# Kernel tuning notes

Hardware: AMD Instinct MI355X
Metric: run time of the kernel (lower is better)

Reference implementation:

```python
import jax, jax.numpy as jnp
import numpy as np

I = 512   # input_size (acts as the row/batch dim)
H = 512   # hidden_size
T = 256   # time steps
STDV = 1.0 / float(np.sqrt(H))


def setup_inputs() -> dict:
    key = jax.random.key(0)
    ks = jax.random.split(key, 20)
    u = lambda k, shape: jax.random.uniform(k, shape, jnp.float32, -STDV, STDV)
    data = jax.random.normal(ks[0], (6, T, I, 1), jnp.float32)
    data = data.at[1].set((data[1] > 0.0).astype(jnp.float32))  # m: binary observation mask
    data = data.at[2].set(jnp.abs(data[2]))                     # d: nonnegative time deltas
    state = jax.random.normal(ks[1], (I, H), jnp.float32) * 0.1
    return dict(
        data=data, state=state,
        w_dg_x=u(ks[2], (I, 1)), w_dg_h=u(ks[3], (1, H)),
        w_xr=u(ks[4], (1, H)), w_hr=u(ks[5], (H, H)), w_mr=u(ks[6], (1, H)),
        w_xz=u(ks[7], (1, H)), w_hz=u(ks[8], (H, H)), w_mz=u(ks[9], (1, H)),
        w_xh=u(ks[10], (1, H)), w_hh=u(ks[11], (H, H)), w_mh=u(ks[12], (1, H)),
        b_dg_x=u(ks[13], (I, 1)), b_dg_h=u(ks[14], (I, H)),
        b_r=u(ks[15], (I, H)), b_z=u(ks[16], (I, H)), b_h=u(ks[17], (I, H)),
    )


def reference(data, state, w_dg_x, w_dg_h, w_xr, w_hr, w_mr, w_xz, w_hz, w_mz,
              w_xh, w_hh, w_mh, b_dg_x, b_dg_h, b_r, b_z, b_h):
    # GRU-D 'mloss' branch; Dropout layer is identity at inference (training=None).
    def step(h, xs):
        x, m, d, xpie = xs  # each (I, 1)
        gamma_x = jnp.exp(-jax.nn.relu(w_dg_x * d + b_dg_x))        # (I, 1)
        gamma_h = jnp.exp(-jax.nn.relu(d @ w_dg_h + b_dg_h))        # (I, H)
        x = m * x + (1.0 - m) * (gamma_x * xpie)                    # decay-gated imputation
        h = gamma_h * h
        r = jax.nn.sigmoid(x @ w_xr + h @ w_hr + m @ w_mr + b_r)    # (I, H)
        z = jax.nn.sigmoid(x @ w_xz + h @ w_hz + m @ w_mz + b_z)
        h_tilde = jnp.tanh(x @ w_xh + (r * h) @ w_hh + m @ w_mh + b_h)
        h_new = (1.0 - z) * h + z * h_tilde
        return h_new, h_new

    _, states = jax.lax.scan(step, state, (data[0], data[1], data[2], data[3]))
    return states  # (T, I, H) hidden state per timestep
```

## Files before the change

kernel.cpp:

```cpp
#include <hip/hip_runtime.h>

typedef _Float16 f16;
typedef _Float16 f16x8 __attribute__((ext_vector_type(8)));
typedef float f32x4 __attribute__((ext_vector_type(4)));

#define T_STEPS 256
#define I_DIM   512
#define H_DIM   512
#define TI      (T_STEPS * I_DIM)
#define ROWS    16
#define NPW     32
#define PADC    520
#define MATSZ   262144

__global__ __launch_bounds__(256) void prep_weights(
    const float* __restrict__ w_hr, const float* __restrict__ w_hz,
    const float* __restrict__ w_hh, f16* __restrict__ wf)
{
    int idx = blockIdx.x * 256 + threadIdx.x;
    int mat = idx >> 18;
    int r   = idx & (MATSZ - 1);
    int nt  = r >> 13;
    int r1  = r & 8191;
    int kk  = r1 >> 9;
    int r2  = r1 & 511;
    int l   = r2 >> 3;
    int j   = r2 & 7;
    int k = kk * 32 + ((l >> 4) << 3) + j;
    int n = (nt << 4) + (l & 15);
    const float* W = (mat == 0) ? w_hr : (mat == 1) ? w_hz : w_hh;
    wf[idx] = (f16)W[k * H_DIM + n];
}

__global__ __launch_bounds__(1024) void grud_main(
    const float* __restrict__ data, const float* __restrict__ state,
    const float* __restrict__ w_dg_x, const float* __restrict__ w_dg_h,
    const float* __restrict__ w_xr, const float* __restrict__ w_mr,
    const float* __restrict__ w_xz, const float* __restrict__ w_mz,
    const float* __restrict__ w_xh, const float* __restrict__ w_mh,
    const float* __restrict__ b_dg_x, const float* __restrict__ b_dg_h,
    const float* __restrict__ b_r, const float* __restrict__ b_z,
    const float* __restrict__ b_h,
    const f16* __restrict__ wf, float* __restrict__ out)
{
    __shared__ f16 hdec_l[ROWS][PADC];
    __shared__ f16 rh_l[ROWS][PADC];

    const int tid = threadIdx.x;
    const int w   = tid >> 6;
    const int l   = tid & 63;
    const int lhi = l >> 4;
    const int llo = l & 15;
    const int n0  = w * NPW;
    const int rowbase = blockIdx.x * ROWS;

    const f16* wfr = wf + (size_t)(2 * w) * 8192;
    const f16* wfz = wfr + MATSZ;
    const f16* wfh = wfr + 2 * MATSZ;

    float h_reg[4][2];
    float hdec[4][2];
    float zreg[4][2];
    float ximp[4], mval[4];

#pragma unroll
    for (int reg = 0; reg < 4; ++reg) {
        int gi = rowbase + lhi * 4 + reg;
#pragma unroll
        for (int c = 0; c < 2; ++c)
            h_reg[reg][c] = state[(size_t)gi * H_DIM + n0 + llo + 16 * c];
    }

    for (int t = 0; t < T_STEPS; ++t) {
#pragma unroll
        for (int reg = 0; reg < 4; ++reg) {
            int i  = lhi * 4 + reg;
            int gi = rowbase + i;
            float d  = data[2 * TI + t * I_DIM + gi];
            float m  = data[1 * TI + t * I_DIM + gi];
            float x  = data[0 * TI + t * I_DIM + gi];
            float xp = data[3 * TI + t * I_DIM + gi];
            float gx = __expf(-fmaxf(w_dg_x[gi] * d + b_dg_x[gi], 0.0f));
            ximp[reg] = m * x + (1.0f - m) * (gx * xp);
            mval[reg] = m;
#pragma unroll
            for (int c = 0; c < 2; ++c) {
                int n = n0 + llo + 16 * c;
                float gh = __expf(-fmaxf(d * w_dg_h[n] + b_dg_h[(size_t)gi * H_DIM + n], 0.0f));
                float hd = gh * h_reg[reg][c];
                hdec[reg][c] = hd;
                hdec_l[i][n] = (f16)hd;
            }
        }
        __syncthreads();

        f32x4 acc_r0 = {0.f,0.f,0.f,0.f}, acc_r1 = {0.f,0.f,0.f,0.f};
        f32x4 acc_z0 = {0.f,0.f,0.f,0.f}, acc_z1 = {0.f,0.f,0.f,0.f};
#pragma unroll
        for (int kk = 0; kk < 16; ++kk) {
            f16x8 a = *(const f16x8*)&hdec_l[llo][kk * 32 + lhi * 8];
            const int fo = (kk * 64 + l) * 8;
            f16x8 br0 = *(const f16x8*)(wfr + fo);
            f16x8 br1 = *(const f16x8*)(wfr + 8192 + fo);
            f16x8 bz0 = *(const f16x8*)(wfz + fo);
            f16x8 bz1 = *(const f16x8*)(wfz + 8192 + fo);
            acc_r0 = __builtin_amdgcn_mfma_f32_16x16x32_f16(a, br0, acc_r0, 0, 0, 0);
            acc_r1 = __builtin_amdgcn_mfma_f32_16x16x32_f16(a, br1, acc_r1, 0, 0, 0);
            acc_z0 = __builtin_amdgcn_mfma_f32_16x16x32_f16(a, bz0, acc_z0, 0, 0, 0);
            acc_z1 = __builtin_amdgcn_mfma_f32_16x16x32_f16(a, bz1, acc_z1, 0, 0, 0);
        }
#pragma unroll
        for (int reg = 0; reg < 4; ++reg) {
            int i  = lhi * 4 + reg;
            int gi = rowbase + i;
#pragma unroll
            for (int c = 0; c < 2; ++c) {
                int n = n0 + llo + 16 * c;
                float sr = (c ? acc_r1[reg] : acc_r0[reg])
                         + ximp[reg] * w_xr[n] + mval[reg] * w_mr[n]
                         + b_r[(size_t)gi * H_DIM + n];
                float rr = 1.0f / (1.0f + __expf(-sr));
                float sz = (c ? acc_z1[reg] : acc_z0[reg])
                         + ximp[reg] * w_xz[n] + mval[reg] * w_mz[n]
                         + b_z[(size_t)gi * H_DIM + n];
                zreg[reg][c] = 1.0f / (1.0f + __expf(-sz));
                rh_l[i][n] = (f16)(rr * hdec[reg][c]);
            }
        }
        __syncthreads();

        f32x4 acc_h0 = {0.f,0.f,0.f,0.f}, acc_h1 = {0.f,0.f,0.f,0.f};
#pragma unroll
        for (int kk = 0; kk < 16; ++kk) {
            f16x8 a = *(const f16x8*)&rh_l[llo][kk * 32 + lhi * 8];
            const int fo = (kk * 64 + l) * 8;
            f16x8 bh0 = *(const f16x8*)(wfh + fo);
            f16x8 bh1 = *(const f16x8*)(wfh + 8192 + fo);
            acc_h0 = __builtin_amdgcn_mfma_f32_16x16x32_f16(a, bh0, acc_h0, 0, 0, 0);
            acc_h1 = __builtin_amdgcn_mfma_f32_16x16x32_f16(a, bh1, acc_h1, 0, 0, 0);
        }
#pragma unroll
        for (int reg = 0; reg < 4; ++reg) {
            int gi = rowbase + lhi * 4 + reg;
#pragma unroll
            for (int c = 0; c < 2; ++c) {
                int n = n0 + llo + 16 * c;
                float sh = (c ? acc_h1[reg] : acc_h0[reg])
                         + ximp[reg] * w_xh[n] + mval[reg] * w_mh[n]
                         + b_h[(size_t)gi * H_DIM + n];
                float e  = __expf(2.0f * sh);
                float th = 1.0f - 2.0f / (e + 1.0f);
                float hn = (1.0f - zreg[reg][c]) * hdec[reg][c] + zreg[reg][c] * th;
                h_reg[reg][c] = hn;
                out[((size_t)t * I_DIM + gi) * H_DIM + n] = hn;
            }
        }
    }
}

extern "C" void kernel_launch(void* const* d_in, const int* in_sizes, int n_in,
                              void* d_out, int out_size, void* d_ws, size_t ws_size,
                              hipStream_t stream) {
    const float* data   = (const float*)d_in[0];
    const float* state  = (const float*)d_in[1];
    const float* w_dg_x = (const float*)d_in[2];
    const float* w_dg_h = (const float*)d_in[3];
    const float* w_xr   = (const float*)d_in[4];
    const float* w_hr   = (const float*)d_in[5];
    const float* w_mr   = (const float*)d_in[6];
    const float* w_xz   = (const float*)d_in[7];
    const float* w_hz   = (const float*)d_in[8];
    const float* w_mz   = (const float*)d_in[9];
    const float* w_xh   = (const float*)d_in[10];
    const float* w_hh   = (const float*)d_in[11];
    const float* w_mh   = (const float*)d_in[12];
    const float* b_dg_x = (const float*)d_in[13];
    const float* b_dg_h = (const float*)d_in[14];
    const float* b_r    = (const float*)d_in[15];
    const float* b_z    = (const float*)d_in[16];
    const float* b_h    = (const float*)d_in[17];
    f16* wf = (f16*)d_ws;
    float* out = (float*)d_out;

    prep_weights<<<3072, 256, 0, stream>>>(w_hr, w_hz, w_hh, wf);
    grud_main<<<32, 1024, 0, stream>>>(data, state, w_dg_x, w_dg_h,
        w_xr, w_mr, w_xz, w_mz, w_xh, w_mh,
        b_dg_x, b_dg_h, b_r, b_z, b_h, wf, out);
}
```

Before: 11.86 ms.

## Split GRU-D hidden columns across 256 blocks with flag-based inter-block sync

```diff
diff --git a/kernel.cpp b/kernel.cpp
--- a/kernel.cpp
+++ b/kernel.cpp
@@ -1,17 +1,30 @@
 #include <hip/hip_runtime.h>
 
 typedef _Float16 f16;
+typedef _Float16 f16x2 __attribute__((ext_vector_type(2)));
 typedef _Float16 f16x8 __attribute__((ext_vector_type(8)));
 typedef float f32x4 __attribute__((ext_vector_type(4)));
+typedef unsigned int uint32;
 
 #define T_STEPS 256
 #define I_DIM   512
 #define H_DIM   512
 #define TI      (T_STEPS * I_DIM)
+#define MATSZ   262144
 #define ROWS    16
-#define NPW     32
+#define COLS    64
 #define PADC    520
-#define MATSZ   262144
+#define NBLK    256
+
+#define WF_BYTES  (3 * MATSZ * 2)
+#define HX_OFF    WF_BYTES
+#define HX_BYTES  (2 * NBLK * ROWS * COLS * 4)
+#define RHX_OFF   (HX_OFF + HX_BYTES)
+#define RHX_BYTES (2 * NBLK * (ROWS/2) * COLS * 4)
+#define FLAG_OFF  (RHX_OFF + RHX_BYTES)
+#define FLAG_INTS (NBLK * 2 * 16)
+
+#define SCOPE_AGENT __HIP_MEMORY_SCOPE_AGENT
 
 __global__ __launch_bounds__(256) void prep_weights(
     const float* __restrict__ w_hr, const float* __restrict__ w_hz,
@@ -32,7 +45,21 @@
     wf[idx] = (f16)W[k * H_DIM + n];
 }
 
-__global__ __launch_bounds__(1024) void grud_main(
+__global__ __launch_bounds__(256) void init_flags(int* flags)
+{
+    for (int i = threadIdx.x; i < FLAG_INTS; i += 256) flags[i] = 0;
+}
+
+__device__ inline void spin_ge(int* f, int tgt)
+{
+    long guard = 0;
+    while (__hip_atomic_load(f, __ATOMIC_ACQUIRE, SCOPE_AGENT) < tgt) {
+        __builtin_amdgcn_s_sleep(8);
+        if (++guard > 500000) break;
+    }
+}
+
+__global__ __launch_bounds__(256, 1) void grud_main(
     const float* __restrict__ data, const float* __restrict__ state,
     const float* __restrict__ w_dg_x, const float* __restrict__ w_dg_h,
     const float* __restrict__ w_xr, const float* __restrict__ w_mr,
@@ -41,120 +68,214 @@
     const float* __restrict__ b_dg_x, const float* __restrict__ b_dg_h,
     const float* __restrict__ b_r, const float* __restrict__ b_z,
     const float* __restrict__ b_h,
-    const f16* __restrict__ wf, float* __restrict__ out)
+    char* __restrict__ ws, float* __restrict__ out)
 {
-    __shared__ f16 hdec_l[ROWS][PADC];
-    __shared__ f16 rh_l[ROWS][PADC];
+    const f16*   wf   = (const f16*)ws;
+    float*       hxf  = (float*)(ws + HX_OFF);
+    uint32*      rhx  = (uint32*)(ws + RHX_OFF);
+    int*         flags= (int*)(ws + FLAG_OFF);
+
+    __shared__ f16   a_l[ROWS][PADC];
+    __shared__ float hdecf[ROWS][COLS + 4];
+    __shared__ float wdh_l[H_DIM];
+    __shared__ float wcol[6][COLS];
+    __shared__ float brl[ROWS][COLS + 4], bzl[ROWS][COLS + 4], bhl[ROWS][COLS + 4];
+    __shared__ float dvl[ROWS], ximpl[ROWS], mvl[ROWS];
+    __shared__ float wdx_l[ROWS], bdx_l[ROWS];
 
     const int tid = threadIdx.x;
-    const int w   = tid >> 6;
+    const int wv  = tid >> 6;
     const int l   = tid & 63;
     const int lhi = l >> 4;
     const int llo = l & 15;
-    const int n0  = w * NPW;
-    const int rowbase = blockIdx.x * ROWS;
-
-    const f16* wfr = wf + (size_t)(2 * w) * 8192;
-    const f16* wfz = wfr + MATSZ;
-    const f16* wfh = wfr + 2 * MATSZ;
-
-    float h_reg[4][2];
-    float hdec[4][2];
-    float zreg[4][2];
-    float ximp[4], mval[4];
-
-#pragma unroll
-    for (int reg = 0; reg < 4; ++reg) {
-        int gi = rowbase + lhi * 4 + reg;
-#pragma unroll
-        for (int c = 0; c < 2; ++c)
-            h_reg[reg][c] = state[(size_t)gi * H_DIM + n0 + llo + 16 * c];
-    }
+    const int rg  = blockIdx.x >> 3;
+    const int cg  = blockIdx.x & 7;
+    const int rowbase = rg * ROWS;
+    const int s_own   = blockIdx.x;
+    int* flag_h_own  = flags + (s_own * 2 + 0) * 16;
+    int* flag_rh_own = flags + (s_own * 2 + 1) * 16;
+
+    f16x8 wr[16], wz[16], wh[16];
+    {
+        const f16* wfb = wf + (size_t)(cg * 4 + wv) * 8192;
+#pragma unroll
+        for (int kk = 0; kk < 16; ++kk) {
+            wr[kk] = *(const f16x8*)(wfb + (kk * 64 + l) * 8);
+            wz[kk] = *(const f16x8*)(wfb + MATSZ + (kk * 64 + l) * 8);
+            wh[kk] = *(const f16x8*)(wfb + 2 * MATSZ + (kk * 64 + l) * 8);
+        }
+    }
+
+    for (int idx = tid; idx < H_DIM; idx += 256) wdh_l[idx] = w_dg_h[idx];
+    for (int idx = tid; idx < 6 * COLS; idx += 256) {
+        int mat = idx >> 6, c = idx & 63;
+        const float* src = (mat == 0) ? w_xr : (mat == 1) ? w_mr : (mat == 2) ? w_xz
+                          : (mat == 3) ? w_mz : (mat == 4) ? w_xh : w_mh;
+        wcol[mat][c] = src[cg * 64 + c];
+    }
+    for (int idx = tid; idx < 3 * ROWS * COLS; idx += 256) {
+        int which = idx >> 10, r = (idx >> 6) & 15, c = idx & 63;
+        const float* src = (which == 0) ? b_r : (which == 1) ? b_z : b_h;
+        float v = src[(size_t)(rowbase + r) * H_DIM + cg * 64 + c];
+        if (which == 0) brl[r][c] = v; else if (which == 1) bzl[r][c] = v; else bhl[r][c] = v;
+    }
+    if (tid < ROWS) {
+        wdx_l[tid] = w_dg_x[rowbase + tid];
+        bdx_l[tid] = b_dg_x[rowbase + tid];
+    }
+    __syncthreads();
+
+    const int di = tid & 15;
+    const int dq = tid >> 4;
+
+    float zsave[4];
 
     for (int t = 0; t < T_STEPS; ++t) {
-#pragma unroll
-        for (int reg = 0; reg < 4; ++reg) {
-            int i  = lhi * 4 + reg;
-            int gi = rowbase + i;
-            float d  = data[2 * TI + t * I_DIM + gi];
-            float m  = data[1 * TI + t * I_DIM + gi];
-            float x  = data[0 * TI + t * I_DIM + gi];
+        if (tid == 0 && t > 0) {
+            __threadfence();
+            __hip_atomic_store(flag_h_own, t, __ATOMIC_RELEASE, SCOPE_AGENT);
+            for (int p = 1; p < 8; ++p) {
+                int cgp = (cg + p) & 7;
+                spin_ge(flags + ((rg * 8 + cgp) * 2 + 0) * 16, t);
+            }
+        }
+        if (tid >= 16 && tid < 32) {
+            int i2 = tid - 16;
+            int gi = rowbase + i2;
+            float dd = data[2 * TI + t * I_DIM + gi];
+            float mm = data[1 * TI + t * I_DIM + gi];
+            float xx = data[0 * TI + t * I_DIM + gi];
             float xp = data[3 * TI + t * I_DIM + gi];
-            float gx = __expf(-fmaxf(w_dg_x[gi] * d + b_dg_x[gi], 0.0f));
-            ximp[reg] = m * x + (1.0f - m) * (gx * xp);
-            mval[reg] = m;
-#pragma unroll
-            for (int c = 0; c < 2; ++c) {
-                int n = n0 + llo + 16 * c;
-                float gh = __expf(-fmaxf(d * w_dg_h[n] + b_dg_h[(size_t)gi * H_DIM + n], 0.0f));
-                float hd = gh * h_reg[reg][c];
-                hdec[reg][c] = hd;
-                hdec_l[i][n] = (f16)hd;
-            }
-        }
-        __syncthreads();
-
-        f32x4 acc_r0 = {0.f,0.f,0.f,0.f}, acc_r1 = {0.f,0.f,0.f,0.f};
-        f32x4 acc_z0 = {0.f,0.f,0.f,0.f}, acc_z1 = {0.f,0.f,0.f,0.f};
+            float gx = __expf(-fmaxf(wdx_l[i2] * dd + bdx_l[i2], 0.0f));
+            dvl[i2] = dd; mvl[i2] = mm;
+            ximpl[i2] = mm * xx + (1.0f - mm) * gx * xp;
+        }
+        __syncthreads();
+
+        {
+            float dd = dvl[di];
+#pragma unroll
+            for (int half = 0; half < 2; ++half) {
+                int k0 = dq * 32 + half * 16;
+                int cgp = k0 >> 6, nb = k0 & 63;
+                float hv[16];
+                if (t == 0) {
+                    const float* sp = state + (size_t)(rowbase + di) * H_DIM + k0;
+#pragma unroll
+                    for (int j = 0; j < 16; ++j) hv[j] = sp[j];
+                } else {
+                    float* hp = hxf + ((size_t)(t & 1) * NBLK + rg * 8 + cgp) * 1024 + di * 64 + nb;
+#pragma unroll
+                    for (int j = 0; j < 16; ++j)
+                        hv[j] = __hip_atomic_load(hp + j, __ATOMIC_RELAXED, SCOPE_AGENT);
+                }
+                const float* bp = b_dg_h + (size_t)(rowbase + di) * H_DIM + k0;
+                f16 hd[16];
+                bool own = (cgp == cg);
+#pragma unroll
+                for (int j = 0; j < 16; ++j) {
+                    float g = __expf(-fmaxf(dd * wdh_l[k0 + j] + bp[j], 0.0f));
+                    float hdv = g * hv[j];
+                    hd[j] = (f16)hdv;
+                    if (own) hdecf[di][nb + j] = hdv;
+                }
+                f16x8 v0, v1;
+#pragma unroll
+                for (int j = 0; j < 8; ++j) { v0[j] = hd[j]; v1[j] = hd[8 + j]; }
+                *(f16x8*)&a_l[di][k0] = v0;
+                *(f16x8*)&a_l[di][k0 + 8] = v1;
+            }
+        }
+        __syncthreads();
+
+        f32x4 ar = {0.f, 0.f, 0.f, 0.f}, az = {0.f, 0.f, 0.f, 0.f};
 #pragma unroll
         for (int kk = 0; kk < 16; ++kk) {
-            f16x8 a = *(const f16x8*)&hdec_l[llo][kk * 32 + lhi * 8];
-            const int fo = (kk * 64 + l) * 8;
-            f16x8 br0 = *(const f16x8*)(wfr + fo);
-            f16x8 br1 = *(const f16x8*)(wfr + 8192 + fo);
-            f16x8 bz0 = *(const f16x8*)(wfz + fo);
-            f16x8 bz1 = *(const f16x8*)(wfz + 8192 + fo);
-            acc_r0 = __builtin_amdgcn_mfma_f32_16x16x32_f16(a, br0, acc_r0, 0, 0, 0);
-            acc_r1 = __builtin_amdgcn_mfma_f32_16x16x32_f16(a, br1, acc_r1, 0, 0, 0);
-            acc_z0 = __builtin_amdgcn_mfma_f32_16x16x32_f16(a, bz0, acc_z0, 0, 0, 0);
-            acc_z1 = __builtin_amdgcn_mfma_f32_16x16x32_f16(a, bz1, acc_z1, 0, 0, 0);
-        }
-#pragma unroll
-        for (int reg = 0; reg < 4; ++reg) {
-            int i  = lhi * 4 + reg;
-            int gi = rowbase + i;
-#pragma unroll
-            for (int c = 0; c < 2; ++c) {
-                int n = n0 + llo + 16 * c;
-                float sr = (c ? acc_r1[reg] : acc_r0[reg])
-                         + ximp[reg] * w_xr[n] + mval[reg] * w_mr[n]
-                         + b_r[(size_t)gi * H_DIM + n];
+            f16x8 a = *(const f16x8*)&a_l[llo][kk * 32 + lhi * 8];
+            ar = __builtin_amdgcn_mfma_f32_16x16x32_f16(a, wr[kk], ar, 0, 0, 0);
+            az = __builtin_amdgcn_mfma_f32_16x16x32_f16(a, wz[kk], az, 0, 0, 0);
+        }
+        {
+            const int n = (wv << 4) + llo;
+            uint32* rslice = rhx + ((size_t)(t & 1) * NBLK + s_own) * 512;
+            float rh[4];
+#pragma unroll
+            for (int reg = 0; reg < 4; ++reg) {
+                int i = 4 * lhi + reg;
+                float sr = ar[reg] + ximpl[i] * wcol[0][n] + mvl[i] * wcol[1][n] + brl[i][n];
                 float rr = 1.0f / (1.0f + __expf(-sr));
-                float sz = (c ? acc_z1[reg] : acc_z0[reg])
-                         + ximp[reg] * w_xz[n] + mval[reg] * w_mz[n]
-                         + b_z[(size_t)gi * H_DIM + n];
-                zreg[reg][c] = 1.0f / (1.0f + __expf(-sz));
-                rh_l[i][n] = (f16)(rr * hdec[reg][c]);
-            }
-        }
-        __syncthreads();
-
-        f32x4 acc_h0 = {0.f,0.f,0.f,0.f}, acc_h1 = {0.f,0.f,0.f,0.f};
+                float sz = az[reg] + ximpl[i] * wcol[2][n] + mvl[i] * wcol[3][n] + bzl[i][n];
+                zsave[reg] = 1.0f / (1.0f + __expf(-sz));
+                rh[reg] = rr * hdecf[i][n];
+            }
+#pragma unroll
+            for (int b = 0; b < 2; ++b) {
+                f16x2 p; p.x = (f16)rh[2 * b]; p.y = (f16)rh[2 * b + 1];
+                __hip_atomic_store(rslice + (2 * lhi + b) * 64 + n,
+                                   __builtin_bit_cast(uint32, p), __ATOMIC_RELAXED, SCOPE_AGENT);
+            }
+        }
+        __syncthreads();
+
+        if (tid == 0) {
+            __threadfence();
+            __hip_atomic_store(flag_rh_own, t + 1, __ATOMIC_RELEASE, SCOPE_AGENT);
+            for (int p = 1; p < 8; ++p) {
+                int cgp = (cg + p) & 7;
+                spin_ge(flags + ((rg * 8 + cgp) * 2 + 1) * 16, t + 1);
+            }
+        }
+        __syncthreads();
+
+        {
+            int cgp = tid >> 5, j = tid & 31;
+            int rp = j >> 2, n0 = (j & 3) * 16;
+            const uint32* src = rhx + ((size_t)(t & 1) * NBLK + rg * 8 + cgp) * 512 + rp * 64 + n0;
+            f16 lo[16], hi[16];
+#pragma unroll
+            for (int jj = 0; jj < 16; ++jj) {
+                uint32 u = __hip_atomic_load((uint32*)(src + jj), __ATOMIC_RELAXED, SCOPE_AGENT);
+                f16x2 p = __builtin_bit_cast(f16x2, u);
+                lo[jj] = p.x; hi[jj] = p.y;
+            }
+            int k0 = cgp * 64 + n0;
+            f16x8 v0, v1, v2, v3;
+#pragma unroll
+            for (int jj = 0; jj < 8; ++jj) {
+                v0[jj] = lo[jj]; v1[jj] = lo[8 + jj];
+                v2[jj] = hi[jj]; v3[jj] = hi[8 + jj];
+            }
+            *(f16x8*)&a_l[2 * rp][k0]     = v0;
+            *(f16x8*)&a_l[2 * rp][k0 + 8] = v1;
+            *(f16x8*)&a_l[2 * rp + 1][k0]     = v2;
+            *(f16x8*)&a_l[2 * rp + 1][k0 + 8] = v3;
+        }
+        __syncthreads();
+
+        f32x4 ah = {0.f, 0.f, 0.f, 0.f};
 #pragma unroll
         for (int kk = 0; kk < 16; ++kk) {
-            f16x8 a = *(const f16x8*)&rh_l[llo][kk * 32 + lhi * 8];
-            const int fo = (kk * 64 + l) * 8;
-            f16x8 bh0 = *(const f16x8*)(wfh + fo);
-            f16x8 bh1 = *(const f16x8*)(wfh + 8192 + fo);
-            acc_h0 = __builtin_amdgcn_mfma_f32_16x16x32_f16(a, bh0, acc_h0, 0, 0, 0);
-            acc_h1 = __builtin_amdgcn_mfma_f32_16x16x32_f16(a, bh1, acc_h1, 0, 0, 0);
-        }
-#pragma unroll
-        for (int reg = 0; reg < 4; ++reg) {
-            int gi = rowbase + lhi * 4 + reg;
-#pragma unroll
-            for (int c = 0; c < 2; ++c) {
-                int n = n0 + llo + 16 * c;
-                float sh = (c ? acc_h1[reg] : acc_h0[reg])
-                         + ximp[reg] * w_xh[n] + mval[reg] * w_mh[n]
-                         + b_h[(size_t)gi * H_DIM + n];
+            f16x8 a = *(const f16x8*)&a_l[llo][kk * 32 + lhi * 8];
+            ah = __builtin_amdgcn_mfma_f32_16x16x32_f16(a, wh[kk], ah, 0, 0, 0);
+        }
+        {
+            const int n = (wv << 4) + llo;
+            const int gcol = cg * 64 + n;
+            float* hslice = hxf + ((size_t)((t + 1) & 1) * NBLK + s_own) * 1024;
+#pragma unroll
+            for (int reg = 0; reg < 4; ++reg) {
+                int i = 4 * lhi + reg;
+                int gi = rowbase + i;
+                float sh = ah[reg] + ximpl[i] * wcol[4][n] + mvl[i] * wcol[5][n] + bhl[i][n];
                 float e  = __expf(2.0f * sh);
                 float th = 1.0f - 2.0f / (e + 1.0f);
-                float hn = (1.0f - zreg[reg][c]) * hdec[reg][c] + zreg[reg][c] * th;
-                h_reg[reg][c] = hn;
-                out[((size_t)t * I_DIM + gi) * H_DIM + n] = hn;
-            }
-        }
+                float hd = hdecf[i][n];
+                float hn = (1.0f - zsave[reg]) * hd + zsave[reg] * th;
+                __builtin_nontemporal_store(hn, &out[((size_t)t * I_DIM + gi) * H_DIM + gcol]);
+                __hip_atomic_store(hslice + i * 64 + n, hn, __ATOMIC_RELAXED, SCOPE_AGENT);
+            }
+        }
+        __syncthreads();
     }
 }
 
@@ -179,11 +300,12 @@
     const float* b_r    = (const float*)d_in[15];
     const float* b_z    = (const float*)d_in[16];
     const float* b_h    = (const float*)d_in[17];
-    f16* wf = (f16*)d_ws;
+    char* ws = (char*)d_ws;
     float* out = (float*)d_out;
 
-    prep_weights<<<3072, 256, 0, stream>>>(w_hr, w_hz, w_hh, wf);
-    grud_main<<<32, 1024, 0, stream>>>(data, state, w_dg_x, w_dg_h,
+    prep_weights<<<3072, 256, 0, stream>>>(w_hr, w_hz, w_hh, (f16*)ws);
+    init_flags<<<1, 256, 0, stream>>>((int*)(ws + FLAG_OFF));
+    grud_main<<<NBLK, 256, 0, stream>>>(data, state, w_dg_x, w_dg_h,
         w_xr, w_mr, w_xz, w_mz, w_xh, w_mh,
-        b_dg_x, b_dg_h, b_r, b_z, b_h, wf, out);
-}
+        b_dg_x, b_dg_h, b_r, b_z, b_h, ws, out);
+}
```

Result: slower. 14.21 ms (+19.9%).
